# Kernel tuning notes

Measured on AMD Instinct MI355X. Metric: run time of the kernel, lower is better.

## Reference

```python
import jax, jax.numpy as jnp
import numpy as np

# Static problem dims (all graphs equal-sized so adaptive pool = uniform bins)
B = 64          # graphs
N = 2048        # nodes per graph
E = 16          # node_emb_dim
H_OUT, W_OUT = 32, 4   # AdaptiveAvgPool2d output -> pooled_dim = 128
COND = 64       # cond_emb_dim
HID = 512       # mlp_h_dim
BN_EPS = 1e-5


def _lin_init(key, out_d, in_d):
    kw, kb = jax.random.split(key)
    lim = 1.0 / np.sqrt(in_d)
    W = jax.random.uniform(kw, (out_d, in_d), jnp.float32, -lim, lim)
    b = jax.random.uniform(kb, (out_d,), jnp.float32, -lim, lim)
    return W, b


def setup_inputs() -> dict:
    key = jax.random.key(0)
    ks = jax.random.split(key, 6)
    Ntot = B * N
    x = jax.random.normal(ks[0], (Ntot, E), jnp.float32)
    batch = jnp.repeat(jnp.arange(B, dtype=jnp.int32), N)  # sorted segment ids
    cond = jax.random.normal(ks[1], (Ntot, COND), jnp.float32)
    mlp_in = COND + H_OUT * W_OUT  # 192
    W1, b1 = _lin_init(ks[2], HID, mlp_in)
    W2, b2 = _lin_init(ks[3], HID, HID)
    W3, b3 = _lin_init(ks[4], 3, HID)
    g1 = jnp.ones((HID,), jnp.float32); be1 = jnp.zeros((HID,), jnp.float32)
    g2 = jnp.ones((HID,), jnp.float32); be2 = jnp.zeros((HID,), jnp.float32)
    return {"x": x, "batch": batch, "conditioner_z_ref": cond,
            "W1": W1, "b1": b1, "g1": g1, "be1": be1,
            "W2": W2, "b2": b2, "g2": g2, "be2": be2,
            "W3": W3, "b3": b3}


def _bn_gelu(h, g, be):
    # BatchNorm1d in training mode: biased batch stats over the node axis
    m = h.mean(axis=0)
    v = h.var(axis=0)
    h = g * (h - m) * jax.lax.rsqrt(v + BN_EPS) + be
    return jax.nn.gelu(h, approximate=False)


def reference(x, batch, conditioner_z_ref, W1, b1, g1, be1, W2, b2, g2, be2, W3, b3):
    # Per-graph adaptive avg pool: since N % H_OUT == 0 and E % W_OUT == 0,
    # AdaptiveAvgPool2d is exactly mean over uniform (N/H_OUT, E/W_OUT) bins.
    xb = x.reshape(B, H_OUT, N // H_OUT, W_OUT, E // W_OUT)
    batch_pooled = xb.mean(axis=(2, 4)).reshape(B, H_OUT * W_OUT)  # [B, 128]
    pooled_per_node = batch_pooled[batch]                           # gather to [Ntot, 128]
    h = jnp.concatenate([conditioner_z_ref, pooled_per_node], axis=1)  # [Ntot, 192]
    h = _bn_gelu(h @ W1.T + b1, g1, be1)
    h = _bn_gelu(h @ W2.T + b2, g2, be2)
    return h @ W3.T + b3  # [Ntot, 3] predicted coords
```

## Files before the change

kernel.cpp:

```cpp
#include <hip/hip_runtime.h>
#include <hip/hip_bf16.h>
#include <math.h>
#include <stdint.h>

#define B_GRAPHS 64
#define N_NODES  2048
#define E_DIM    16
#define M_TOT    (B_GRAPHS * N_NODES)
#define K_COND   64
#define MLP_IN   192
#define HID      512
#define POOLD    128
#define BN_EPS   1e-5f

typedef __attribute__((ext_vector_type(8))) short bfrag8;
typedef __attribute__((ext_vector_type(4))) float facc4;

__device__ __forceinline__ unsigned short f2b(float f) {
    unsigned int x = __builtin_bit_cast(unsigned int, f);
    unsigned int r = x + 0x7fffu + ((x >> 16) & 1u);
    return (unsigned short)(r >> 16);
}
__device__ __forceinline__ float b2f(unsigned short u) {
    unsigned int x = ((unsigned int)u) << 16;
    return __builtin_bit_cast(float, x);
}

__device__ __forceinline__ float gelu_fast(float y) {
    float x  = y * 0.70710678118654752440f;
    float ax = fabsf(x);
    float t  = __builtin_amdgcn_rcpf(fmaf(0.3275911f, ax, 1.0f));
    float p  = fmaf(1.061405429f, t, -1.453152027f);
    p = fmaf(p, t, 1.421413741f);
    p = fmaf(p, t, -0.284496736f);
    p = fmaf(p, t, 0.254829592f);
    p = p * t;
    float e = __expf(-x * x);
    float erfax = fmaf(-p, e, 1.0f);
    float erfx  = copysignf(erfax, x);
    return 0.5f * y * (1.0f + erfx);
}

#define GLOAD_LDS16(g, l)                                                        \
    __builtin_amdgcn_global_load_lds(                                            \
        (const __attribute__((address_space(1))) unsigned int*)(const void*)(g), \
        (__attribute__((address_space(3))) unsigned int*)(void*)(l), 16, 0, 0)

__global__ __launch_bounds__(512) void prep_kernel(const float* __restrict__ x,
                                                   const float* __restrict__ W1,
                                                   const float* __restrict__ b1,
                                                   float* __restrict__ gbias) {
    __shared__ float pl[POOLD];
    int g = blockIdx.x, t = threadIdx.x;
    if (t < 128) {
        int h = t >> 2, w = t & 3;
        const float* base = x + (size_t)g * N_NODES * E_DIM + (size_t)h * 64 * E_DIM + w * 4;
        float s = 0.f;
        #pragma unroll 4
        for (int r = 0; r < 64; ++r) {
            float4 v = *reinterpret_cast<const float4*>(base + (size_t)r * E_DIM);
            s += v.x + v.y + v.z + v.w;
        }
        pl[h * 4 + w] = s * (1.0f / 256.0f);
    }
    __syncthreads();
    const float* wr_ = W1 + (size_t)t * MLP_IN + K_COND;
    float s = b1[t];
    #pragma unroll 4
    for (int k = 0; k < POOLD; ++k) s = fmaf(pl[k], wr_[k], s);
    gbias[g * HID + t] = s;
}

__global__ __launch_bounds__(256) void cvt_kernel(const float* __restrict__ s,
                                                  unsigned short* __restrict__ d) {
    size_t i = ((size_t)blockIdx.x * 256 + threadIdx.x) * 8;
    float4 v0 = *reinterpret_cast<const float4*>(s + i);
    float4 v1 = *reinterpret_cast<const float4*>(s + i + 4);
    unsigned short t[8] = {f2b(v0.x), f2b(v0.y), f2b(v0.z), f2b(v0.w),
                           f2b(v1.x), f2b(v1.y), f2b(v1.z), f2b(v1.w)};
    *reinterpret_cast<bfrag8*>(d + i) = *reinterpret_cast<bfrag8*>(t);
}

__device__ __forceinline__ bfrag8 load_f32x8_as_bf16(const float* p) {
    float4 v0 = *reinterpret_cast<const float4*>(p);
    float4 v1 = *reinterpret_cast<const float4*>(p + 4);
    unsigned short t[8] = {f2b(v0.x), f2b(v0.y), f2b(v0.z), f2b(v0.w),
                           f2b(v1.x), f2b(v1.y), f2b(v1.z), f2b(v1.w)};
    return *reinterpret_cast<bfrag8*>(t);
}

__global__ __launch_bounds__(512, 1) void gemm1_kernel(const float* __restrict__ A,
                                                       const float* __restrict__ W,
                                                       const float* __restrict__ gbias,
                                                       float* __restrict__ sums,
                                                       unsigned short* __restrict__ C) {
    __shared__ float sArr[HID], qArr[HID];
    const int t = threadIdx.x;
    const int r0 = blockIdx.x * 128;
    const int g = r0 >> 11;
    const int l = t & 63, w = t >> 6;
    const int wr = w >> 2, wc = w & 3;
    const int ln = l & 15, kg = l >> 4;
    sArr[t] = 0.f; qArr[t] = 0.f;
    __syncthreads();

    facc4 acc[4][8];
    const facc4 z = {0.f, 0.f, 0.f, 0.f};
    #pragma unroll
    for (int a = 0; a < 4; ++a)
        #pragma unroll
        for (int b = 0; b < 8; ++b) acc[a][b] = z;

    #pragma unroll
    for (int ks = 0; ks < 2; ++ks) {
        bfrag8 af[4], bf[8];
        #pragma unroll
        for (int a = 0; a < 4; ++a)
            af[a] = load_f32x8_as_bf16(A + (size_t)(r0 + wr * 64 + a * 16 + ln) * K_COND + ks * 32 + kg * 8);
        #pragma unroll
        for (int b = 0; b < 8; ++b)
            bf[b] = load_f32x8_as_bf16(W + (size_t)(wc * 128 + b * 16 + ln) * MLP_IN + ks * 32 + kg * 8);
        #pragma unroll
        for (int a = 0; a < 4; ++a)
            #pragma unroll
            for (int b = 0; b < 8; ++b)
                acc[a][b] = __builtin_amdgcn_mfma_f32_16x16x32_bf16(af[a], bf[b], acc[a][b], 0, 0, 0);
    }

    const float* gb = gbias + (size_t)g * HID;
    float gbv[8];
    #pragma unroll
    for (int b = 0; b < 8; ++b) gbv[b] = gb[wc * 128 + b * 16 + ln];
    float cs[8], cq[8];
    #pragma unroll
    for (int b = 0; b < 8; ++b) { cs[b] = 0.f; cq[b] = 0.f; }
    #pragma unroll
    for (int a = 0; a < 4; ++a) {
        #pragma unroll
        for (int i = 0; i < 4; ++i) {
            size_t rbase = (size_t)(r0 + wr * 64 + a * 16 + kg * 4 + i) * HID + wc * 128 + ln;
            #pragma unroll
            for (int b = 0; b < 8; ++b) {
                float v = acc[a][b][i] + gbv[b];
                C[rbase + b * 16] = f2b(v);
                cs[b] += v; cq[b] = fmaf(v, v, cq[b]);
            }
        }
    }
    #pragma unroll
    for (int b = 0; b < 8; ++b) {
        cs[b] += __shfl_xor(cs[b], 16, 64); cq[b] += __shfl_xor(cq[b], 16, 64);
        cs[b] += __shfl_xor(cs[b], 32, 64); cq[b] += __shfl_xor(cq[b], 32, 64);
    }
    if (kg == 0) {
        #pragma unroll
        for (int b = 0; b < 8; ++b) {
            int cl = wc * 128 + b * 16 + ln;
            atomicAdd(&sArr[cl], cs[b]); atomicAdd(&qArr[cl], cq[b]);
        }
    }
    __syncthreads();
    atomicAdd(&sums[t], sArr[t]);
    atomicAdd(&sums[HID + t], qArr[t]);
}

__global__ __launch_bounds__(512, 1) void gemm2_kernel(const unsigned short* __restrict__ A,
                                                       const unsigned short* __restrict__ Bm,
                                                       const float* __restrict__ sums1,
                                                       const float* __restrict__ g1,
                                                       const float* __restrict__ be1,
                                                       const float* __restrict__ bias,
                                                       float* __restrict__ sums,
                                                       unsigned short* __restrict__ C) {
    __shared__ unsigned short As[2][128 * 32];
    __shared__ unsigned short Bs[3][512 * 32];
    __shared__ float lss[2 * HID];
    __shared__ float sArr[HID], qArr[HID];
    const int t = threadIdx.x;
    const int r0 = blockIdx.x * 128;
    const int l = t & 63, w = t >> 6;
    const int wr = w >> 2, wc = w & 3;
    const int ln = l & 15, kg = l >> 4;
    const int arow = t >> 2, aslot = t & 3;
    const int awslot = aslot ^ ((arow >> 1) & 3);
    const int rr = l >> 2, sp = l & 3;
    const int bss = sp ^ ((rr >> 1) & 3);

    {
        float mean = sums1[t] * (1.0f / M_TOT);
        float var  = sums1[HID + t] * (1.0f / M_TOT) - mean * mean;
        float sc   = g1[t] * rsqrtf(var + BN_EPS);
        lss[t] = sc;
        lss[HID + t] = be1[t] - mean * sc;
    }
    sArr[t] = 0.f; qArr[t] = 0.f;

    facc4 acc[4][8];
    const facc4 z = {0.f, 0.f, 0.f, 0.f};
    #pragma unroll
    for (int a = 0; a < 4; ++a)
        #pragma unroll
        for (int b = 0; b < 8; ++b) acc[a][b] = z;

    const unsigned short* aptr = A + (size_t)(r0 + arow) * HID + aslot * 8;

    auto actwrite = [&](bfrag8 va, int kk, unsigned short* asb) {
        unsigned short tmp[8];
        #pragma unroll
        for (int j = 0; j < 8; ++j) {
            int col = kk + aslot * 8 + j;
            float xv = b2f((unsigned short)va[j]);
            tmp[j] = f2b(gelu_fast(fmaf(xv, lss[col], lss[HID + col])));
        }
        *reinterpret_cast<bfrag8*>(&asb[arow * 32 + awslot * 8]) = *reinterpret_cast<bfrag8*>(tmp);
    };
    auto stageB = [&](int kk, unsigned short* bsb) {
        #pragma unroll
        for (int c = 0; c < 4; ++c) {
            int chunk = w * 4 + c;
            const unsigned short* gb = Bm + (size_t)(chunk * 16 + rr) * HID + kk + bss * 8;
            GLOAD_LDS16(gb, &bsb[chunk * 512]);
        }
    };

    __syncthreads();

    bfrag8 va_p, va_q;
    va_p = *reinterpret_cast<const bfrag8*>(aptr);
    stageB(0, Bs[0]);
    va_q = *reinterpret_cast<const bfrag8*>(aptr + 32);
    stageB(32, Bs[1]);
    asm volatile("s_waitcnt vmcnt(9)" ::: "memory");
    actwrite(va_p, 0, As[0]);
    va_p = va_q;
    asm volatile("s_waitcnt lgkmcnt(0)" ::: "memory");

    unsigned short* bs_r  = Bs[0];
    unsigned short* bs_n1 = Bs[1];
    unsigned short* bs_n2 = Bs[2];
    unsigned short* as_r  = As[0];
    unsigned short* as_w  = As[1];

    for (int tt = 0; tt < 16; ++tt) {
        if (tt < 15) asm volatile("s_waitcnt vmcnt(4)" ::: "memory");
        else         asm volatile("s_waitcnt vmcnt(0)" ::: "memory");
        __builtin_amdgcn_s_barrier();
        if (tt < 14) {
            va_q = *reinterpret_cast<const bfrag8*>(aptr + (tt + 2) * 32);
            stageB((tt + 2) * 32, bs_n2);
        }
        bfrag8 af[4], bf[8];
        #pragma unroll
        for (int a = 0; a < 4; ++a) {
            int RA = wr * 64 + a * 16 + ln;
            af[a] = *reinterpret_cast<const bfrag8*>(&as_r[RA * 32 + (kg ^ ((RA >> 1) & 3)) * 8]);
        }
        #pragma unroll
        for (int b = 0; b < 8; ++b) {
            int RB = wc * 128 + b * 16 + ln;
            bf[b] = *reinterpret_cast<const bfrag8*>(&bs_r[RB * 32 + (kg ^ ((RB >> 1) & 3)) * 8]);
        }
        if (tt < 15) actwrite(va_p, (tt + 1) * 32, as_w);
        __builtin_amdgcn_s_setprio(1);
        #pragma unroll
        for (int a = 0; a < 4; ++a)
            #pragma unroll
            for (int b = 0; b < 8; ++b)
                acc[a][b] = __builtin_amdgcn_mfma_f32_16x16x32_bf16(af[a], bf[b], acc[a][b], 0, 0, 0);
        __builtin_amdgcn_s_setprio(0);
        asm volatile("s_waitcnt lgkmcnt(0)" ::: "memory");
        va_p = va_q;
        unsigned short* tmpb = bs_r; bs_r = bs_n1; bs_n1 = bs_n2; bs_n2 = tmpb;
        unsigned short* tmpa = as_r; as_r = as_w; as_w = tmpa;
    }

    float bb[8];
    #pragma unroll
    for (int b = 0; b < 8; ++b) bb[b] = bias[wc * 128 + b * 16 + ln];
    float cs[8], cq[8];
    #pragma unroll
    for (int b = 0; b < 8; ++b) { cs[b] = 0.f; cq[b] = 0.f; }
    #pragma unroll
    for (int a = 0; a < 4; ++a) {
        #pragma unroll
        for (int i = 0; i < 4; ++i) {
            size_t rbase = (size_t)(r0 + wr * 64 + a * 16 + kg * 4 + i) * HID + wc * 128 + ln;
            #pragma unroll
            for (int b = 0; b < 8; ++b) {
                float v = acc[a][b][i] + bb[b];
                C[rbase + b * 16] = f2b(v);
                cs[b] += v; cq[b] = fmaf(v, v, cq[b]);
            }
        }
    }
    #pragma unroll
    for (int b = 0; b < 8; ++b) {
        cs[b] += __shfl_xor(cs[b], 16, 64); cq[b] += __shfl_xor(cq[b], 16, 64);
        cs[b] += __shfl_xor(cs[b], 32, 64); cq[b] += __shfl_xor(cq[b], 32, 64);
    }
    if (kg == 0) {
        #pragma unroll
        for (int b = 0; b < 8; ++b) {
            int cl = wc * 128 + b * 16 + ln;
            atomicAdd(&sArr[cl], cs[b]); atomicAdd(&qArr[cl], cq[b]);
        }
    }
    __syncthreads();
    atomicAdd(&sums[t], sArr[t]);
    atomicAdd(&sums[HID + t], qArr[t]);
}

__global__ void finalize_kernel(const float* __restrict__ sums, const float* __restrict__ g,
                                const float* __restrict__ be, float* __restrict__ ss) {
    int n = threadIdx.x;
    float mean = sums[n] * (1.0f / M_TOT);
    float var = sums[HID + n] * (1.0f / M_TOT) - mean * mean;
    float sc = g[n] * rsqrtf(var + BN_EPS);
    ss[n] = sc;
    ss[HID + n] = be[n] - mean * sc;
}

__global__ __launch_bounds__(256) void g3_kernel(const unsigned short* __restrict__ H2,
                                                 const float* __restrict__ ss2,
                                                 const float* __restrict__ W3,
                                                 const float* __restrict__ b3,
                                                 float* __restrict__ out) {
    __shared__ float lss[2 * HID];
    __shared__ float lw3[3 * HID];
    int t = threadIdx.x;
    for (int i = t; i < 2 * HID; i += 256) lss[i] = ss2[i];
    for (int i = t; i < 3 * HID; i += 256) lw3[i] = W3[i];
    __syncthreads();
    int l = t & 63, w = t >> 6;
    int rsub = l >> 3, lk = l & 7;
    int row = blockIdx.x * 32 + w * 8 + rsub;
    const unsigned short* p = H2 + (size_t)row * HID;
    float o0 = 0.f, o1 = 0.f, o2 = 0.f;
    #pragma unroll
    for (int it = 0; it < 8; ++it) {
        int k = it * 64 + lk * 8;
        bfrag8 v = *reinterpret_cast<const bfrag8*>(p + k);
        #pragma unroll
        for (int j = 0; j < 8; ++j) {
            float x = b2f((unsigned short)v[j]);
            float y = fmaf(x, lss[k + j], lss[HID + k + j]);
            y = gelu_fast(y);
            o0 = fmaf(y, lw3[k + j], o0);
            o1 = fmaf(y, lw3[HID + k + j], o1);
            o2 = fmaf(y, lw3[2 * HID + k + j], o2);
        }
    }
    #pragma unroll
    for (int m = 1; m < 8; m <<= 1) {
        o0 += __shfl_xor(o0, m, 64);
        o1 += __shfl_xor(o1, m, 64);
        o2 += __shfl_xor(o2, m, 64);
    }
    if (lk == 0) {
        out[(size_t)row * 3 + 0] = o0 + b3[0];
        out[(size_t)row * 3 + 1] = o1 + b3[1];
        out[(size_t)row * 3 + 2] = o2 + b3[2];
    }
}

extern "C" void kernel_launch(void* const* d_in, const int* in_sizes, int n_in,
                              void* d_out, int out_size, void* d_ws, size_t ws_size,
                              hipStream_t stream) {
    const float* x     = (const float*)d_in[0];
    const float* cond  = (const float*)d_in[2];
    const float* W1    = (const float*)d_in[3];
    const float* b1    = (const float*)d_in[4];
    const float* g1    = (const float*)d_in[5];
    const float* be1   = (const float*)d_in[6];
    const float* W2    = (const float*)d_in[7];
    const float* b2    = (const float*)d_in[8];
    const float* g2    = (const float*)d_in[9];
    const float* be2   = (const float*)d_in[10];
    const float* W3    = (const float*)d_in[11];
    const float* b3    = (const float*)d_in[12];

    const size_t H_BYTES = (size_t)M_TOT * HID * 2;
    if (ws_size < 2 * H_BYTES) return;
    char* ws = (char*)d_ws;
    unsigned short* H1 = (unsigned short*)ws;
    unsigned short* H2 = (unsigned short*)(ws + H_BYTES);

    float* outf   = (float*)d_out;
    float* gbias  = outf;
    float* sums1  = gbias + B_GRAPHS * HID;
    float* sums2  = sums1 + 2 * HID;
    unsigned short* W2bf = (unsigned short*)(sums2 + 2 * HID);
    float* ss2 = (float*)ws;

    hipMemsetAsync(sums1, 0, 2 * 2 * HID * sizeof(float), stream);

    prep_kernel<<<B_GRAPHS, 512, 0, stream>>>(x, W1, b1, gbias);
    cvt_kernel<<<(HID * HID / 8) / 256, 256, 0, stream>>>(W2, W2bf);

    gemm1_kernel<<<dim3(M_TOT / 128, 1), 512, 0, stream>>>(
        cond, W1, gbias, sums1, H1);

    gemm2_kernel<<<dim3(M_TOT / 128, 1), 512, 0, stream>>>(
        H1, W2bf, sums1, g1, be1, b2, sums2, H2);

    finalize_kernel<<<1, HID, 0, stream>>>(sums2, g2, be2, ss2);

    g3_kernel<<<M_TOT / 32, 256, 0, stream>>>(H2, ss2, W3, b3, outf);
}
```

Measured before the change: 291.9 us.

## Stage full activated A tile in LDS and stream W2 fragments from global

gemm2 now applies BN+GELU to the whole 128x512 A tile up front and stores it in one XOR-swizzled 128 KB LDS buffer. The pipelined LDS staging of W2 (global_load_lds, triple buffering, barriers per k-step) is removed, and B fragments are now loaded straight from global/L2 into registers with one-step prefetch. gemm1 similarly loads its A tile into swizzled LDS with coalesced reads and preloads W fragments. This removes per-step barriers and LDS traffic for B. In exchange, global load latency is exposed on every k-step, GELU work no longer overlaps with MFMA, and the large LDS allocation caps occupancy.

```diff
diff --git a/kernel.cpp b/kernel.cpp
--- a/kernel.cpp
+++ b/kernel.cpp
@@ -40,11 +40,6 @@
     float erfx  = copysignf(erfax, x);
     return 0.5f * y * (1.0f + erfx);
 }
-
-#define GLOAD_LDS16(g, l)                                                        \
-    __builtin_amdgcn_global_load_lds(                                            \
-        (const __attribute__((address_space(1))) unsigned int*)(const void*)(g), \
-        (__attribute__((address_space(3))) unsigned int*)(void*)(l), 16, 0, 0)
 
 __global__ __launch_bounds__(512) void prep_kernel(const float* __restrict__ x,
                                                    const float* __restrict__ W1,
@@ -94,6 +89,7 @@
                                                        const float* __restrict__ gbias,
                                                        float* __restrict__ sums,
                                                        unsigned short* __restrict__ C) {
+    __shared__ unsigned short As[128 * 64];
     __shared__ float sArr[HID], qArr[HID];
     const int t = threadIdx.x;
     const int r0 = blockIdx.x * 128;
@@ -102,6 +98,24 @@
     const int wr = w >> 2, wc = w & 3;
     const int ln = l & 15, kg = l >> 4;
     sArr[t] = 0.f; qArr[t] = 0.f;
+
+    {
+        const int cg = t & 7, rb = t >> 3;
+        #pragma unroll
+        for (int i = 0; i < 2; ++i) {
+            int row = rb + i * 64;
+            bfrag8 vv = load_f32x8_as_bf16(A + (size_t)(r0 + row) * K_COND + cg * 8);
+            int dg = row * 8 + (cg ^ (row & 7));
+            *reinterpret_cast<bfrag8*>(&As[dg * 8]) = vv;
+        }
+    }
+    bfrag8 bf0[8], bf1[8];
+    #pragma unroll
+    for (int b = 0; b < 8; ++b) {
+        int RB = wc * 128 + b * 16 + ln;
+        bf0[b] = load_f32x8_as_bf16(W + (size_t)RB * MLP_IN + kg * 8);
+        bf1[b] = load_f32x8_as_bf16(W + (size_t)RB * MLP_IN + 32 + kg * 8);
+    }
     __syncthreads();
 
     facc4 acc[4][8];
@@ -112,19 +126,19 @@
         for (int b = 0; b < 8; ++b) acc[a][b] = z;
 
     #pragma unroll
-    for (int ks = 0; ks < 2; ++ks) {
-        bfrag8 af[4], bf[8];
+    for (int s = 0; s < 2; ++s) {
+        bfrag8 af[4];
+        #pragma unroll
+        for (int a = 0; a < 4; ++a) {
+            int RA = wr * 64 + a * 16 + ln;
+            af[a] = *reinterpret_cast<const bfrag8*>(&As[(RA * 8 + ((s * 4 + kg) ^ (RA & 7))) * 8]);
+        }
         #pragma unroll
         for (int a = 0; a < 4; ++a)
-            af[a] = load_f32x8_as_bf16(A + (size_t)(r0 + wr * 64 + a * 16 + ln) * K_COND + ks * 32 + kg * 8);
-        #pragma unroll
-        for (int b = 0; b < 8; ++b)
-            bf[b] = load_f32x8_as_bf16(W + (size_t)(wc * 128 + b * 16 + ln) * MLP_IN + ks * 32 + kg * 8);
-        #pragma unroll
-        for (int a = 0; a < 4; ++a)
             #pragma unroll
             for (int b = 0; b < 8; ++b)
-                acc[a][b] = __builtin_amdgcn_mfma_f32_16x16x32_bf16(af[a], bf[b], acc[a][b], 0, 0, 0);
+                acc[a][b] = __builtin_amdgcn_mfma_f32_16x16x32_bf16(
+                    af[a], s == 0 ? bf0[b] : bf1[b], acc[a][b], 0, 0, 0);
     }
 
     const float* gb = gbias + (size_t)g * HID;
@@ -172,28 +186,59 @@
                                                        const float* __restrict__ bias,
                                                        float* __restrict__ sums,
                                                        unsigned short* __restrict__ C) {
-    __shared__ unsigned short As[2][128 * 32];
-    __shared__ unsigned short Bs[3][512 * 32];
-    __shared__ float lss[2 * HID];
+    __shared__ unsigned short As[128 * 512];
     __shared__ float sArr[HID], qArr[HID];
     const int t = threadIdx.x;
     const int r0 = blockIdx.x * 128;
     const int l = t & 63, w = t >> 6;
     const int wr = w >> 2, wc = w & 3;
     const int ln = l & 15, kg = l >> 4;
-    const int arow = t >> 2, aslot = t & 3;
-    const int awslot = aslot ^ ((arow >> 1) & 3);
-    const int rr = l >> 2, sp = l & 3;
-    const int bss = sp ^ ((rr >> 1) & 3);
-
+
+    sArr[t] = 0.f; qArr[t] = 0.f;
+
+    const int cg = t & 63;
+    const int cb = cg * 8;
+    float sc[8], sh[8];
     {
-        float mean = sums1[t] * (1.0f / M_TOT);
-        float var  = sums1[HID + t] * (1.0f / M_TOT) - mean * mean;
-        float sc   = g1[t] * rsqrtf(var + BN_EPS);
-        lss[t] = sc;
-        lss[HID + t] = be1[t] - mean * sc;
-    }
-    sArr[t] = 0.f; qArr[t] = 0.f;
+        const float inv = 1.0f / (float)M_TOT;
+        #pragma unroll
+        for (int j = 0; j < 8; ++j) {
+            float m_ = sums1[cb + j] * inv;
+            float v_ = sums1[HID + cb + j] * inv - m_ * m_;
+            float scv = g1[cb + j] * rsqrtf(v_ + BN_EPS);
+            sc[j] = scv;
+            sh[j] = be1[cb + j] - m_ * scv;
+        }
+    }
+
+    {
+        const int rb = t >> 6;
+        bfrag8 v[16];
+        #pragma unroll
+        for (int i = 0; i < 16; ++i) {
+            int row = rb + i * 8;
+            v[i] = *reinterpret_cast<const bfrag8*>(&A[(size_t)(r0 + row) * HID + cb]);
+        }
+        #pragma unroll
+        for (int i = 0; i < 16; ++i) {
+            int row = rb + i * 8;
+            unsigned short tmp[8];
+            #pragma unroll
+            for (int j = 0; j < 8; ++j) {
+                float xv = b2f((unsigned short)v[i][j]);
+                tmp[j] = f2b(gelu_fast(fmaf(xv, sc[j], sh[j])));
+            }
+            int dg = row * 64 + (cg ^ (row & 7));
+            *reinterpret_cast<bfrag8*>(&As[dg * 8]) = *reinterpret_cast<bfrag8*>(tmp);
+        }
+    }
+    bfrag8 bfc[8], bfn[8];
+    #pragma unroll
+    for (int b = 0; b < 8; ++b) {
+        int RB = wc * 128 + b * 16 + ln;
+        bfc[b] = *reinterpret_cast<const bfrag8*>(&Bm[(size_t)RB * HID + kg * 8]);
+    }
+    __syncthreads();
 
     facc4 acc[4][8];
     const facc4 z = {0.f, 0.f, 0.f, 0.f};
@@ -202,76 +247,30 @@
         #pragma unroll
         for (int b = 0; b < 8; ++b) acc[a][b] = z;
 
-    const unsigned short* aptr = A + (size_t)(r0 + arow) * HID + aslot * 8;
-
-    auto actwrite = [&](bfrag8 va, int kk, unsigned short* asb) {
-        unsigned short tmp[8];
-        #pragma unroll
-        for (int j = 0; j < 8; ++j) {
-            int col = kk + aslot * 8 + j;
-            float xv = b2f((unsigned short)va[j]);
-            tmp[j] = f2b(gelu_fast(fmaf(xv, lss[col], lss[HID + col])));
-        }
-        *reinterpret_cast<bfrag8*>(&asb[arow * 32 + awslot * 8]) = *reinterpret_cast<bfrag8*>(tmp);
-    };
-    auto stageB = [&](int kk, unsigned short* bsb) {
-        #pragma unroll
-        for (int c = 0; c < 4; ++c) {
-            int chunk = w * 4 + c;
-            const unsigned short* gb = Bm + (size_t)(chunk * 16 + rr) * HID + kk + bss * 8;
-            GLOAD_LDS16(gb, &bsb[chunk * 512]);
-        }
-    };
-
-    __syncthreads();
-
-    bfrag8 va_p, va_q;
-    va_p = *reinterpret_cast<const bfrag8*>(aptr);
-    stageB(0, Bs[0]);
-    va_q = *reinterpret_cast<const bfrag8*>(aptr + 32);
-    stageB(32, Bs[1]);
-    asm volatile("s_waitcnt vmcnt(9)" ::: "memory");
-    actwrite(va_p, 0, As[0]);
-    va_p = va_q;
-    asm volatile("s_waitcnt lgkmcnt(0)" ::: "memory");
-
-    unsigned short* bs_r  = Bs[0];
-    unsigned short* bs_n1 = Bs[1];
-    unsigned short* bs_n2 = Bs[2];
-    unsigned short* as_r  = As[0];
-    unsigned short* as_w  = As[1];
-
-    for (int tt = 0; tt < 16; ++tt) {
-        if (tt < 15) asm volatile("s_waitcnt vmcnt(4)" ::: "memory");
-        else         asm volatile("s_waitcnt vmcnt(0)" ::: "memory");
-        __builtin_amdgcn_s_barrier();
-        if (tt < 14) {
-            va_q = *reinterpret_cast<const bfrag8*>(aptr + (tt + 2) * 32);
-            stageB((tt + 2) * 32, bs_n2);
-        }
-        bfrag8 af[4], bf[8];
+    #pragma unroll
+    for (int s = 0; s < 16; ++s) {
+        if (s < 15) {
+            #pragma unroll
+            for (int b = 0; b < 8; ++b) {
+                int RB = wc * 128 + b * 16 + ln;
+                bfn[b] = *reinterpret_cast<const bfrag8*>(
+                    &Bm[(size_t)RB * HID + (s + 1) * 32 + kg * 8]);
+            }
+        }
+        bfrag8 af[4];
         #pragma unroll
         for (int a = 0; a < 4; ++a) {
             int RA = wr * 64 + a * 16 + ln;
-            af[a] = *reinterpret_cast<const bfrag8*>(&as_r[RA * 32 + (kg ^ ((RA >> 1) & 3)) * 8]);
-        }
-        #pragma unroll
-        for (int b = 0; b < 8; ++b) {
-            int RB = wc * 128 + b * 16 + ln;
-            bf[b] = *reinterpret_cast<const bfrag8*>(&bs_r[RB * 32 + (kg ^ ((RB >> 1) & 3)) * 8]);
-        }
-        if (tt < 15) actwrite(va_p, (tt + 1) * 32, as_w);
-        __builtin_amdgcn_s_setprio(1);
+            af[a] = *reinterpret_cast<const bfrag8*>(
+                &As[(RA * 64 + ((s * 4 + kg) ^ (RA & 7))) * 8]);
+        }
         #pragma unroll
         for (int a = 0; a < 4; ++a)
             #pragma unroll
             for (int b = 0; b < 8; ++b)
-                acc[a][b] = __builtin_amdgcn_mfma_f32_16x16x32_bf16(af[a], bf[b], acc[a][b], 0, 0, 0);
-        __builtin_amdgcn_s_setprio(0);
-        asm volatile("s_waitcnt lgkmcnt(0)" ::: "memory");
-        va_p = va_q;
-        unsigned short* tmpb = bs_r; bs_r = bs_n1; bs_n1 = bs_n2; bs_n2 = tmpb;
-        unsigned short* tmpa = as_r; as_r = as_w; as_w = tmpa;
+                acc[a][b] = __builtin_amdgcn_mfma_f32_16x16x32_bf16(af[a], bfc[b], acc[a][b], 0, 0, 0);
+        #pragma unroll
+        for (int b = 0; b < 8; ++b) bfc[b] = bfn[b];
     }
 
     float bb[8];
```

Result: slower. 336.1 us (+15.1%).
